# Performance work log

Hardware: AMD Instinct MI355X
Metric: run time of the kernel (lower is better)

Reference implementation:

```python
import jax, jax.numpy as jnp
import numpy as np

T = 15          # fixed window length from docstring
CENTER = 7      # center_idx
MAXL = 8        # max_len_f = max_len_b = 8
B, D, H = 8192, 512, 512


def _gru_final(x, lengths, Wih, Whh, bih, bhh):
    """Run a GRU over x (B, L, D) and return the hidden state after each
    sample's own `lengths` steps (packed-sequence final-hidden semantics)."""
    Bn, L, _ = x.shape
    Hn = Whh.shape[1]
    # Precompute input projections for all timesteps: (B, L, 3H)
    xp = jnp.einsum('bld,gd->blg', x, Wih) + bih
    mask = jnp.arange(L)[None, :] < lengths[:, None]  # (B, L) valid steps

    def step(h, inp):
        xp_t, m_t = inp                      # (B,3H), (B,)
        gh = h @ Whh.T + bhh                 # (B,3H)
        xr, xz, xn = jnp.split(xp_t, 3, axis=-1)
        hr, hz, hn = jnp.split(gh, 3, axis=-1)
        r = jax.nn.sigmoid(xr + hr)
        z = jax.nn.sigmoid(xz + hz)
        n = jnp.tanh(xn + r * hn)
        h_new = (1.0 - z) * n + z * h
        h = jnp.where(m_t[:, None], h_new, h)  # freeze h past sequence end
        return h, None

    h0 = jnp.zeros((Bn, Hn), x.dtype)
    hT, _ = jax.lax.scan(step, h0, (jnp.moveaxis(xp, 0, 1)[:L], mask.T))
    return hT


def setup_inputs() -> dict:
    key = jax.random.key(0)
    ks = jax.random.split(key, 16)
    s_ih = 1.0 / np.sqrt(H)
    u = lambda k, shape: jax.random.uniform(k, shape, jnp.float32, -s_ih, s_ih)
    inp = {
        'padded_window': jax.random.normal(ks[0], (B, T, D), jnp.float32),
        'window_len': jax.random.randint(ks[1], (B,), 1, T + 1, jnp.int32),
        # forward GRU params (PyTorch layout: gates ordered r,z,n)
        'Wih_f': u(ks[2], (3 * H, D)), 'Whh_f': u(ks[3], (3 * H, H)),
        'bih_f': u(ks[4], (3 * H,)),   'bhh_f': u(ks[5], (3 * H,)),
        # backward GRU params
        'Wih_b': u(ks[6], (3 * H, D)), 'Whh_b': u(ks[7], (3 * H, H)),
        'bih_b': u(ks[8], (3 * H,)),   'bhh_b': u(ks[9], (3 * H,)),
        # MLP: Linear(2H,H) -> ReLU -> Linear(H,H)
        'W1': u(ks[10], (H, 2 * H)), 'b1': u(ks[11], (H,)),
        'W2': u(ks[12], (H, H)),     'b2': u(ks[13], (H,)),
    }
    return inp


def reference(padded_window, window_len, Wih_f, Whh_f, bih_f, bhh_f,
              Wih_b, Whh_b, bih_b, bhh_b, W1, b1, W2, b2):
    len_f = (window_len - 1) // 2 + 1   # (B,)
    len_b = window_len // 2 + 1         # (B,)
    j = jnp.arange(MAXL)
    # forward sub-sequence: window[center-l_f+1 : center+1]
    idx_f = jnp.clip(CENTER - len_f[:, None] + 1 + j[None, :], 0, T - 1)
    # backward sub-sequence: flip(window[center : center+l_b]) -> descending idx
    idx_b = jnp.clip(CENTER + len_b[:, None] - 1 - j[None, :], 0, T - 1)
    xf = jnp.take_along_axis(padded_window, idx_f[:, :, None], axis=1)  # (B,8,D)
    xb = jnp.take_along_axis(padded_window, idx_b[:, :, None], axis=1)  # (B,8,D)
    h_f = _gru_final(xf, len_f, Wih_f, Whh_f, bih_f, bhh_f)
    h_b = _gru_final(xb, len_b, Wih_b, Whh_b, bih_b, bhh_b)
    combined = jnp.concatenate([h_f, h_b], axis=1)  # (B, 2H)
    hidden = jax.nn.relu(combined @ W1.T + b1)
    return hidden @ W2.T + b2
```

## Files before the change

kernel.cpp:

```cpp
#include <hip/hip_runtime.h>

typedef unsigned short u16;
typedef __attribute__((ext_vector_type(4))) float f32x4;
typedef __attribute__((ext_vector_type(8))) __bf16 bf16x8;
typedef __attribute__((ext_vector_type(8))) u16 u16x8;
typedef __attribute__((ext_vector_type(4))) u16 u16x4;
typedef __attribute__((ext_vector_type(4))) int i32x4;

#define MFMA(a, b, c) __builtin_amdgcn_mfma_f32_16x16x32_bf16(a, b, c, 0, 0, 0)

__device__ __forceinline__ u16 f2bf(float f) {
  union { float f; unsigned u; } v; v.f = f;
  unsigned r = v.u + 0x7FFFu + ((v.u >> 16) & 1u);
  return (u16)(r >> 16);
}
__device__ __forceinline__ float bf2f(u16 b) {
  union { unsigned u; float f; } v; v.u = ((unsigned)b) << 16; return v.f;
}
__device__ __forceinline__ float sigm(float x) { return 1.f / (1.f + __expf(-x)); }
__device__ __forceinline__ float tanh_(float x) {
  float e = __expf(-2.f * fabsf(x));
  float r = (1.f - e) / (1.f + e);
  return x < 0.f ? -r : r;
}

#define GSTRIDE 131072

__global__ __launch_bounds__(256) void cvt_bf16(const float* __restrict__ src,
                                                u16* __restrict__ dst, int n8) {
  int i = blockIdx.x * 256 + threadIdx.x;
  if (i >= n8) return;
  int e = i * 8;
  u16x8 o;
#pragma unroll
  for (int j = 0; j < 8; ++j) o[j] = f2bf(src[e + j]);
  *(u16x8*)(dst + e) = o;
}

#define LROWA 520

__global__ __launch_bounds__(256)
__attribute__((amdgpu_waves_per_eu(1, 1))) void xp_gemm(
    const float* __restrict__ win, const int* __restrict__ wlen,
    const u16* __restrict__ Wihb_f, const u16* __restrict__ Wihb_b,
    const float* __restrict__ bih_f, const float* __restrict__ bih_b,
    const float* __restrict__ bhh_f, const float* __restrict__ bhh_b,
    u16* __restrict__ xp) {
  extern __shared__ char smem[];
  u16* As = (u16*)smem;

  const int dir = blockIdx.y;
  const u16* Wb = dir ? Wihb_b : Wihb_f;
  const float* bih = dir ? bih_b : bih_f;
  const float* bhh = dir ? bhh_b : bhh_f;

  const int tid = threadIdx.x;
  const int bx = blockIdx.x;

  {
    const int r = tid >> 1, hh = tid & 1;
    const int m = bx * 128 + r;
    const int s = m >> 3, tt = m & 7;
    const int wl = wlen[s];
    const int len = dir ? (wl / 2 + 1) : ((wl - 1) / 2 + 1);
    const int widx = dir ? (6 + len - tt) : (8 - len + tt);
    const float* src = win + ((size_t)s * 15 + widx) * 512 + hh * 256;
    u16* dst = As + r * LROWA + hh * 256;
#pragma unroll
    for (int i = 0; i < 32; ++i) {
      f32x4 v0 = *(const f32x4*)(src + i * 8);
      f32x4 v1 = *(const f32x4*)(src + i * 8 + 4);
      u16x8 o;
      o[0] = f2bf(v0[0]); o[1] = f2bf(v0[1]); o[2] = f2bf(v0[2]); o[3] = f2bf(v0[3]);
      o[4] = f2bf(v1[0]); o[5] = f2bf(v1[1]); o[6] = f2bf(v1[2]); o[7] = f2bf(v1[3]);
      *(u16x8*)(dst + i * 8) = o;
    }
  }
  __syncthreads();

  const int wave = tid >> 6;
  const int lane = tid & 63;
  const int ln = lane & 15;
  const int ks = lane >> 4;

#pragma unroll 1
  for (int g = 0; g < 6; ++g) {
    const int c0 = wave * 24 + g * 4;

    f32x4 acc[8][4];
#pragma unroll
    for (int mt = 0; mt < 8; ++mt)
#pragma unroll
      for (int u = 0; u < 4; ++u)
#pragma unroll
        for (int j = 0; j < 4; ++j) acc[mt][u][j] = 0.f;

#pragma unroll
    for (int kk = 0; kk < 16; ++kk) {
      const int krel = kk * 32 + ks * 8;
      bf16x8 a[8];
#pragma unroll
      for (int mt = 0; mt < 8; ++mt)
        a[mt] = *(const bf16x8*)(As + (mt * 16 + ln) * LROWA + krel);
      bf16x8 b[4];
#pragma unroll
      for (int u = 0; u < 4; ++u)
        b[u] = *(const bf16x8*)(Wb + (size_t)((c0 + u) * 16 + ln) * 512 + krel);
#pragma unroll
      for (int mt = 0; mt < 8; ++mt)
#pragma unroll
        for (int u = 0; u < 4; ++u) acc[mt][u] = MFMA(a[mt], b[u], acc[mt][u]);
    }

#pragma unroll
    for (int u = 0; u < 4; ++u) {
      const int col = (c0 + u) * 16 + ln;
      const float bv = bih[col] + (col < 1024 ? bhh[col] : 0.f);
#pragma unroll
      for (int mt = 0; mt < 8; ++mt)
#pragma unroll
        for (int j = 0; j < 4; ++j) {
          const int rowm = bx * 128 + mt * 16 + ks * 4 + j;
          const int s = rowm >> 3, t = rowm & 7;
          const size_t idx = ((size_t)(dir * 8 + t) * 96 + (c0 + u)) * GSTRIDE +
                             (size_t)(s >> 2) * 64 + ln * 4 + (s & 3);
          xp[idx] = f2bf(acc[mt][u][j] + bv);
        }
    }
  }
}

#define LROW 520

__global__ __launch_bounds__(1024)
__attribute__((amdgpu_waves_per_eu(4, 4))) void gru_rec(
    const int* __restrict__ wlen, const u16* __restrict__ Whhb_f,
    const u16* __restrict__ Whhb_b, const float* __restrict__ bhh_f,
    const float* __restrict__ bhh_b, const u16* __restrict__ xp,
    u16* __restrict__ hcat) {
  extern __shared__ char smem[];
  u16* hb0 = (u16*)smem;
  u16* hb1 = hb0 + 64 * LROW;
  int* len_s = (int*)(hb1 + 64 * LROW);
  int* bmax_s = len_s + 64;

  const int dir = blockIdx.x & 1;
  const int grp = blockIdx.x >> 1;
  const int s0 = grp * 64;
  const u16* W = dir ? Whhb_b : Whhb_f;
  const float* bhh = dir ? bhh_b : bhh_f;

  const int tid = threadIdx.x;
  const int wave = tid >> 6;
  const int lane = tid & 63;
  const int ln = lane & 15;
  const int ks = lane >> 4;

  if (tid == 0) *bmax_s = 0;
  for (int i = tid; i < 64 * LROW / 8; i += 1024) ((u16x8*)hb0)[i] = (u16x8)0;
  __syncthreads();
  if (tid < 64) {
    int wl = wlen[s0 + tid];
    int len = dir ? (wl / 2 + 1) : ((wl - 1) / 2 + 1);
    len_s[tid] = len;
    atomicMax(bmax_s, len);
  }
  __syncthreads();
  const int bmax = *bmax_s;

  float b_hn[2];
#pragma unroll
  for (int p = 0; p < 2; ++p) b_hn[p] = bhh[1024 + (p * 16 + wave) * 16 + ln];

  for (int t = 0; t < bmax; ++t) {
    u16* h_cur = (t & 1) ? hb1 : hb0;
    u16* h_nxt = (t & 1) ? hb0 : hb1;
    const u16* xpt = xp + (size_t)(dir * 8 + t) * 96 * GSTRIDE;

#pragma unroll
    for (int p = 0; p < 2; ++p) {
      const int q = p * 16 + wave;
      const int dcol = q * 16 + ln;
      const u16* wrow = W + (size_t)dcol * 512;

      u16x4 xr4[4], xz4[4], xn4[4];
#pragma unroll
      for (int mt = 0; mt < 4; ++mt) {
        const size_t off = (size_t)((s0 >> 2) + mt * 4 + ks) * 64 + ln * 4;
        xr4[mt] = *(const u16x4*)(xpt + (size_t)q * GSTRIDE + off);
        xz4[mt] = *(const u16x4*)(xpt + (size_t)(32 + q) * GSTRIDE + off);
        xn4[mt] = *(const u16x4*)(xpt + (size_t)(64 + q) * GSTRIDE + off);
      }

      f32x4 accr[4], accz[4], acchn[4];
#pragma unroll
      for (int mt = 0; mt < 4; ++mt)
#pragma unroll
        for (int j = 0; j < 4; ++j) {
          accr[mt][j] = 0.f; accz[mt][j] = 0.f; acchn[mt][j] = 0.f;
        }

#pragma unroll
      for (int kk = 0; kk < 16; ++kk) {
        const int krel = kk * 32 + ks * 8;
        bf16x8 a[4];
#pragma unroll
        for (int mt = 0; mt < 4; ++mt)
          a[mt] = *(const bf16x8*)(h_cur + (mt * 16 + ln) * LROW + krel);
        bf16x8 br = *(const bf16x8*)(wrow + krel);
        bf16x8 bz = *(const bf16x8*)(wrow + 512 * 512 + krel);
        bf16x8 bn = *(const bf16x8*)(wrow + 1024 * 512 + krel);
#pragma unroll
        for (int mt = 0; mt < 4; ++mt) {
          accr[mt] = MFMA(a[mt], br, accr[mt]);
          accz[mt] = MFMA(a[mt], bz, accz[mt]);
          acchn[mt] = MFMA(a[mt], bn, acchn[mt]);
        }
      }

#pragma unroll
      for (int mt = 0; mt < 4; ++mt)
#pragma unroll
        for (int j = 0; j < 4; ++j) {
          const int row = mt * 16 + ks * 4 + j;
          float xr = bf2f(xr4[mt][j]);
          float xz = bf2f(xz4[mt][j]);
          float xn = bf2f(xn4[mt][j]);
          float rr = sigm(accr[mt][j] + xr);
          float zz = sigm(accz[mt][j] + xz);
          float nn = tanh_(xn + rr * (acchn[mt][j] + b_hn[p]));
          float hold = bf2f(h_cur[row * LROW + dcol]);
          float hnew = (t < len_s[row]) ? ((1.f - zz) * nn + zz * hold) : hold;
          h_nxt[row * LROW + dcol] = f2bf(hnew);
        }
    }
    __syncthreads();
  }

  const u16* hf = (bmax & 1) ? hb1 : hb0;
  const int xrow = tid >> 4;
  const int xcol = tid & 15;
#pragma unroll
  for (int i = 0; i < 4; ++i) {
    int off = (i * 16 + xcol) * 8;
    u16x8 v = *(const u16x8*)(hf + xrow * LROW + off);
    __builtin_nontemporal_store(
        v, (u16x8*)(hcat + (size_t)(s0 + xrow) * 1024 + dir * 512 + off));
  }
}

__global__ __launch_bounds__(256) void build_wcat(const float* __restrict__ Whh,
                                                  const float* __restrict__ Wih,
                                                  u16* __restrict__ Wcat) {
  int i = blockIdx.x * 256 + threadIdx.x;
  if (i >= 1536 * 1024 / 8) return;
  int e = i * 8;
  int g = e >> 10, k = e & 1023;
  const float* src = (k < 512) ? (Whh + g * 512 + k) : (Wih + g * 512 + (k - 512));
  u16x8 o;
#pragma unroll
  for (int j = 0; j < 8; ++j) o[j] = f2bf(src[j]);
  *(u16x8*)(Wcat + e) = o;
}

__global__ __launch_bounds__(512)
__attribute__((amdgpu_waves_per_eu(2, 2))) void gru_persistent(
    const float* __restrict__ win, const int* __restrict__ wlen,
    const u16* __restrict__ Wcat_f, const u16* __restrict__ Wcat_b,
    const float* __restrict__ bih_f, const float* __restrict__ bhh_f,
    const float* __restrict__ bih_b, const float* __restrict__ bhh_b,
    u16* __restrict__ hcat) {
  extern __shared__ char smem[];
  u16* h_s = (u16*)smem;
  u16* x_s = (u16*)(smem + 64 * LROW * 2);
  int* len_s = (int*)(smem + 2 * 64 * LROW * 2);
  int* bmax_s = len_s + 64;

  const int dir = blockIdx.x & 1;
  const int grp = blockIdx.x >> 1;
  const int s0 = grp * 64;
  const u16* W = dir ? Wcat_b : Wcat_f;
  const float* bih = dir ? bih_b : bih_f;
  const float* bhh = dir ? bhh_b : bhh_f;

  const int tid = threadIdx.x;
  const int wave = tid >> 6;
  const int lane = tid & 63;
  const int ln = lane & 15;
  const int ks = lane >> 4;

  if (tid == 0) *bmax_s = 0;
  for (int i = tid; i < 64 * LROW / 8; i += 512) ((u16x8*)h_s)[i] = (u16x8)0;
  __syncthreads();
  if (tid < 64) {
    int wl = wlen[s0 + tid];
    int len = dir ? (wl / 2 + 1) : ((wl - 1) / 2 + 1);
    len_s[tid] = len;
    atomicMax(bmax_s, len);
  }
  __syncthreads();
  const int bmax = *bmax_s;

  float b_r[4], b_z[4], b_xn[4], b_hn[4];
#pragma unroll
  for (int p = 0; p < 4; ++p) {
    int d = (p * 8 + wave) * 16 + ln;
    b_r[p] = bih[d] + bhh[d];
    b_z[p] = bih[512 + d] + bhh[512 + d];
    b_xn[p] = bih[1024 + d];
    b_hn[p] = bhh[1024 + d];
  }

  const int xrow = tid >> 3;
  const int xcol = tid & 7;
  const int mylen = len_s[xrow];
  const long xbase = (long)(s0 + xrow) * 15 + (dir ? (6 + mylen) : (8 - mylen));

  for (int t = 0; t < bmax; ++t) {
    {
      long rowidx = dir ? (xbase - t) : (xbase + t);
      const float* src = win + rowidx * 512;
      u16* dst = x_s + xrow * LROW;
#pragma unroll
      for (int i = 0; i < 8; ++i) {
        int off = xcol * 8 + i * 64;
        f32x4 v0 = *(const f32x4*)(src + off);
        f32x4 v1 = *(const f32x4*)(src + off + 4);
        u16x8 o;
        o[0] = f2bf(v0[0]); o[1] = f2bf(v0[1]); o[2] = f2bf(v0[2]); o[3] = f2bf(v0[3]);
        o[4] = f2bf(v1[0]); o[5] = f2bf(v1[1]); o[6] = f2bf(v1[2]); o[7] = f2bf(v1[3]);
        *(u16x8*)(dst + off) = o;
      }
    }
    __syncthreads();

    unsigned holdp[3][4][2];

#pragma unroll
    for (int p = 0; p < 4; ++p) {
      const int dcol = (p * 8 + wave) * 16 + ln;
      const u16* wrow = W + (size_t)dcol * 1024;

      f32x4 accr[4], accz[4], acchn[4], accxn[4];
#pragma unroll
      for (int mt = 0; mt < 4; ++mt)
#pragma unroll
        for (int j = 0; j < 4; ++j) {
          accr[mt][j] = 0.f; accz[mt][j] = 0.f;
          acchn[mt][j] = 0.f; accxn[mt][j] = 0.f;
        }

#pragma unroll
      for (int kk = 0; kk < 16; ++kk) {
        const int krel = kk * 32 + ks * 8;
        bf16x8 a[4];
#pragma unroll
        for (int mt = 0; mt < 4; ++mt)
          a[mt] = *(const bf16x8*)(h_s + (mt * 16 + ln) * LROW + krel);
        bf16x8 br = *(const bf16x8*)(wrow + krel);
        bf16x8 bz = *(const bf16x8*)(wrow + 512 * 1024 + krel);
        bf16x8 bn = *(const bf16x8*)(wrow + 1024 * 1024 + krel);
#pragma unroll
        for (int mt = 0; mt < 4; ++mt) {
          accr[mt] = MFMA(a[mt], br, accr[mt]);
          accz[mt] = MFMA(a[mt], bz, accz[mt]);
          acchn[mt] = MFMA(a[mt], bn, acchn[mt]);
        }
      }
#pragma unroll
      for (int kk = 0; kk < 16; ++kk) {
        const int krel = kk * 32 + ks * 8;
        bf16x8 a[4];
#pragma unroll
        for (int mt = 0; mt < 4; ++mt)
          a[mt] = *(const bf16x8*)(x_s + (mt * 16 + ln) * LROW + krel);
        bf16x8 br = *(const bf16x8*)(wrow + 512 + krel);
        bf16x8 bz = *(const bf16x8*)(wrow + 512 * 1024 + 512 + krel);
        bf16x8 bn = *(const bf16x8*)(wrow + 1024 * 1024 + 512 + krel);
#pragma unroll
        for (int mt = 0; mt < 4; ++mt) {
          accr[mt] = MFMA(a[mt], br, accr[mt]);
          accz[mt] = MFMA(a[mt], bz, accz[mt]);
          accxn[mt] = MFMA(a[mt], bn, accxn[mt]);
        }
      }

      if (p < 3) {
#pragma unroll
        for (int mt = 0; mt < 4; ++mt)
#pragma unroll
          for (int jp = 0; jp < 2; ++jp) {
            unsigned pk = 0;
#pragma unroll
            for (int jh = 0; jh < 2; ++jh) {
              const int j = jp * 2 + jh;
              const int row = mt * 16 + ks * 4 + j;
              float rr = sigm(accr[mt][j] + b_r[p]);
              float zz = sigm(accz[mt][j] + b_z[p]);
              float nn = tanh_(accxn[mt][j] + b_xn[p] +
                               rr * (acchn[mt][j] + b_hn[p]));
              float hold = bf2f(h_s[row * LROW + dcol]);
              float hnew = (t < len_s[row]) ? ((1.f - zz) * nn + zz * hold) : hold;
              pk |= ((unsigned)f2bf(hnew)) << (16 * jh);
            }
            holdp[p][mt][jp] = pk;
          }
      } else {
        __syncthreads();
#pragma unroll
        for (int pp = 0; pp < 3; ++pp) {
          const int dd = (pp * 8 + wave) * 16 + ln;
#pragma unroll
          for (int mt = 0; mt < 4; ++mt)
#pragma unroll
            for (int jp = 0; jp < 2; ++jp) {
              unsigned pk = holdp[pp][mt][jp];
              const int row = mt * 16 + ks * 4 + jp * 2;
              h_s[row * LROW + dd] = (u16)pk;
              h_s[(row + 1) * LROW + dd] = (u16)(pk >> 16);
            }
        }
#pragma unroll
        for (int mt = 0; mt < 4; ++mt)
#pragma unroll
          for (int j = 0; j < 4; ++j) {
            const int row = mt * 16 + ks * 4 + j;
            float rr = sigm(accr[mt][j] + b_r[3]);
            float zz = sigm(accz[mt][j] + b_z[3]);
            float nn = tanh_(accxn[mt][j] + b_xn[3] +
                             rr * (acchn[mt][j] + b_hn[3]));
            float hold = bf2f(h_s[row * LROW + dcol]);
            float hnew = (t < len_s[row]) ? ((1.f - zz) * nn + zz * hold) : hold;
            h_s[row * LROW + dcol] = f2bf(hnew);
          }
      }
    }
  }

  __syncthreads();
#pragma unroll
  for (int i = 0; i < 8; ++i) {
    int off = xcol * 8 + i * 64;
    u16x8 v = *(const u16x8*)(h_s + xrow * LROW + off);
    __builtin_nontemporal_store(
        v, (u16x8*)(hcat + (size_t)(s0 + xrow) * 1024 + dir * 512 + off));
  }
}

__global__ __launch_bounds__(256) void mlp_gemm(const u16* __restrict__ A,
                                                const u16* __restrict__ Bw,
                                                const float* __restrict__ bias,
                                                void* __restrict__ out, int M,
                                                int N, int K, int mode) {
  __shared__ u16 As[128 * 64], Bs[128 * 64];
  const int tid = threadIdx.x;
  const int wave = tid >> 6, lane = tid & 63;
  const int ln = lane & 15, ks = lane >> 4;
  const int wm = wave & 1, wn = wave >> 1;
  const int m0 = blockIdx.x * 128, n0 = blockIdx.y * 128;
  f32x4 acc[4][4];
#pragma unroll
  for (int mt = 0; mt < 4; ++mt)
#pragma unroll
    for (int nt = 0; nt < 4; ++nt)
#pragma unroll
      for (int j = 0; j < 4; ++j) acc[mt][nt][j] = 0.f;

  const int r = tid >> 1, hh = tid & 1;
  for (int k0 = 0; k0 < K; k0 += 64) {
    const i32x4* sa = (const i32x4*)(A + (size_t)(m0 + r) * K + k0 + hh * 32);
    const i32x4* sb = (const i32x4*)(Bw + (size_t)(n0 + r) * K + k0 + hh * 32);
    i32x4* da = (i32x4*)(As + r * 64 + hh * 32);
    i32x4* db = (i32x4*)(Bs + r * 64 + hh * 32);
#pragma unroll
    for (int i = 0; i < 4; ++i) da[i] = sa[i];
#pragma unroll
    for (int i = 0; i < 4; ++i) db[i] = sb[i];
    __syncthreads();
#pragma unroll
    for (int kk = 0; kk < 2; ++kk) {
      bf16x8 af[4], bfm[4];
#pragma unroll
      for (int mt = 0; mt < 4; ++mt)
        af[mt] = *(const bf16x8*)(As + (wm * 64 + mt * 16 + ln) * 64 + kk * 32 + ks * 8);
#pragma unroll
      for (int nt = 0; nt < 4; ++nt)
        bfm[nt] = *(const bf16x8*)(Bs + (wn * 64 + nt * 16 + ln) * 64 + kk * 32 + ks * 8);
#pragma unroll
      for (int mt = 0; mt < 4; ++mt)
#pragma unroll
        for (int nt = 0; nt < 4; ++nt) acc[mt][nt] = MFMA(af[mt], bfm[nt], acc[mt][nt]);
    }
    __syncthreads();
  }

#pragma unroll
  for (int nt = 0; nt < 4; ++nt) {
    int col = n0 + wn * 64 + nt * 16 + ln;
    float bv = bias[col];
#pragma unroll
    for (int mt = 0; mt < 4; ++mt)
#pragma unroll
      for (int j = 0; j < 4; ++j) {
        int row = m0 + wm * 64 + mt * 16 + ks * 4 + j;
        float v = acc[mt][nt][j] + bv;
        if (mode) {
          v = fmaxf(v, 0.f);
          ((u16*)out)[(size_t)row * N + col] = f2bf(v);
        } else {
          ((float*)out)[(size_t)row * N + col] = v;
        }
      }
  }
}

extern "C" void kernel_launch(void* const* d_in, const int* in_sizes, int n_in,
                              void* d_out, int out_size, void* d_ws, size_t ws_size,
                              hipStream_t stream) {
  (void)in_sizes; (void)n_in; (void)out_size;
  const float* win = (const float*)d_in[0];
  const int* wlen = (const int*)d_in[1];
  const float* Wih_f = (const float*)d_in[2];
  const float* Whh_f = (const float*)d_in[3];
  const float* bih_f = (const float*)d_in[4];
  const float* bhh_f = (const float*)d_in[5];
  const float* Wih_b = (const float*)d_in[6];
  const float* Whh_b = (const float*)d_in[7];
  const float* bih_b = (const float*)d_in[8];
  const float* bhh_b = (const float*)d_in[9];
  const float* W1 = (const float*)d_in[10];
  const float* b1 = (const float*)d_in[11];
  const float* W2 = (const float*)d_in[12];
  const float* b2 = (const float*)d_in[13];

  const size_t NEED = 4ull * 1572864 + 1048576 + 524288 + 16777216 + 8388608 +
                      402653184ull;

  if (ws_size >= NEED) {
    char* ws = (char*)d_ws;
    u16* Whhb_f = (u16*)ws; ws += 1572864;
    u16* Whhb_b = (u16*)ws; ws += 1572864;
    u16* Wihb_f = (u16*)ws; ws += 1572864;
    u16* Wihb_b = (u16*)ws; ws += 1572864;
    u16* W1b = (u16*)ws;    ws += 1048576;
    u16* W2b = (u16*)ws;    ws += 524288;
    u16* hcat = (u16*)ws;   ws += 16777216;
    u16* hidden = (u16*)ws; ws += 8388608;
    u16* xp = (u16*)ws;     ws += 402653184;

    cvt_bf16<<<384, 256, 0, stream>>>(Whh_f, Whhb_f, 98304);
    cvt_bf16<<<384, 256, 0, stream>>>(Whh_b, Whhb_b, 98304);
    cvt_bf16<<<384, 256, 0, stream>>>(Wih_f, Wihb_f, 98304);
    cvt_bf16<<<384, 256, 0, stream>>>(Wih_b, Wihb_b, 98304);
    cvt_bf16<<<256, 256, 0, stream>>>(W1, W1b, 65536);
    cvt_bf16<<<128, 256, 0, stream>>>(W2, W2b, 32768);

    const int SMEM_XP = 128 * LROWA * 2;
    (void)hipFuncSetAttribute((const void*)xp_gemm,
                              hipFuncAttributeMaxDynamicSharedMemorySize, SMEM_XP);
    xp_gemm<<<dim3(512, 2), 256, SMEM_XP, stream>>>(
        win, wlen, Wihb_f, Wihb_b, bih_f, bih_b, bhh_f, bhh_b, xp);

    const int SMEM = 2 * 64 * LROW * 2 + 64 * 4 + 16;
    (void)hipFuncSetAttribute((const void*)gru_rec,
                              hipFuncAttributeMaxDynamicSharedMemorySize, SMEM);
    gru_rec<<<256, 1024, SMEM, stream>>>(wlen, Whhb_f, Whhb_b, bhh_f, bhh_b, xp,
                                         hcat);

    mlp_gemm<<<dim3(64, 4), 256, 0, stream>>>(hcat, W1b, b1, hidden, 8192, 512, 1024, 1);
    mlp_gemm<<<dim3(64, 4), 256, 0, stream>>>(hidden, W2b, b2, d_out, 8192, 512, 512, 0);
  } else {
    char* ws = (char*)d_ws;
    u16* Wcat_f = (u16*)ws;  ws += 3145728;
    u16* Wcat_b = (u16*)ws;  ws += 3145728;
    u16* W1b = (u16*)ws;     ws += 1048576;
    u16* W2b = (u16*)ws;     ws += 524288;
    u16* hcat = (u16*)ws;    ws += 16777216;
    u16* hidden = (u16*)ws;  ws += 8388608;

    build_wcat<<<768, 256, 0, stream>>>(Whh_f, Wih_f, Wcat_f);
    build_wcat<<<768, 256, 0, stream>>>(Whh_b, Wih_b, Wcat_b);
    cvt_bf16<<<256, 256, 0, stream>>>(W1, W1b, 65536);
    cvt_bf16<<<128, 256, 0, stream>>>(W2, W2b, 32768);

    const int SMEM = 2 * 64 * LROW * 2 + 64 * 4 + 16;
    (void)hipFuncSetAttribute((const void*)gru_persistent,
                              hipFuncAttributeMaxDynamicSharedMemorySize, SMEM);
    gru_persistent<<<256, 512, SMEM, stream>>>(win, wlen, Wcat_f, Wcat_b, bih_f,
                                               bhh_f, bih_b, bhh_b, hcat);

    mlp_gemm<<<dim3(64, 4), 256, 0, stream>>>(hcat, W1b, b1, hidden, 8192, 512, 1024, 1);
    mlp_gemm<<<dim3(64, 4), 256, 0, stream>>>(hidden, W2b, b2, d_out, 8192, 512, 512, 0);
  }
}
```

Measured before the change: 1.885 ms.

## Sort samples by length and repack recurrent weights into MFMA fragment order

Adds a counting sort of samples by window length so each GRU block and input-projection block holds samples of similar length. The projection GEMM is reorganised per timestep and skips tiles whose longest sample has already finished, and the recurrence's per-block step count shrinks. The final MLP scatters rows back through the permutation. Separately, Whh is repacked so each wave's B-fragment loads are contiguous and coalesced, at the cost of an extra sort kernel and indirect indexing.

```diff
diff --git a/kernel.cpp b/kernel.cpp
--- a/kernel.cpp
+++ b/kernel.cpp
@@ -37,34 +37,81 @@
   *(u16x8*)(dst + e) = o;
 }
 
+__global__ __launch_bounds__(256) void wrepack(const float* __restrict__ Whh,
+                                               u16* __restrict__ Wp) {
+  int i = blockIdx.x * 256 + threadIdx.x;
+  if (i >= 98304) return;
+  int q = i / 3072;
+  int r1 = i % 3072;
+  int kk = r1 / 192;
+  int r2 = r1 % 192;
+  int g = r2 / 64;
+  int r3 = r2 % 64;
+  int ks = r3 >> 4, ln = r3 & 15;
+  const float* src =
+      Whh + (size_t)(g * 512 + q * 16 + ln) * 512 + kk * 32 + ks * 8;
+  u16x8 o;
+#pragma unroll
+  for (int j = 0; j < 8; ++j) o[j] = f2bf(src[j]);
+  *(u16x8*)(Wp + (size_t)i * 8) = o;
+}
+
+__global__ __launch_bounds__(1024) void sort_len(const int* __restrict__ wlen,
+                                                 int* __restrict__ order) {
+  __shared__ int cnt[16];
+  __shared__ int off[16];
+  const int tid = threadIdx.x;
+  if (tid < 16) cnt[tid] = 0;
+  __syncthreads();
+  for (int i = tid; i < 8192; i += 1024) atomicAdd(&cnt[wlen[i] - 1], 1);
+  __syncthreads();
+  if (tid == 0) {
+    int run = 0;
+#pragma unroll
+    for (int b = 0; b < 15; ++b) { off[b] = run; run += cnt[b]; }
+  }
+  __syncthreads();
+  for (int i = tid; i < 8192; i += 1024) {
+    int pos = atomicAdd(&off[wlen[i] - 1], 1);
+    order[pos] = i;
+  }
+}
+
 #define LROWA 520
 
 __global__ __launch_bounds__(256)
 __attribute__((amdgpu_waves_per_eu(1, 1))) void xp_gemm(
     const float* __restrict__ win, const int* __restrict__ wlen,
-    const u16* __restrict__ Wihb_f, const u16* __restrict__ Wihb_b,
-    const float* __restrict__ bih_f, const float* __restrict__ bih_b,
-    const float* __restrict__ bhh_f, const float* __restrict__ bhh_b,
-    u16* __restrict__ xp) {
+    const int* __restrict__ order, const u16* __restrict__ Wihb_f,
+    const u16* __restrict__ Wihb_b, const float* __restrict__ bih_f,
+    const float* __restrict__ bih_b, const float* __restrict__ bhh_f,
+    const float* __restrict__ bhh_b, u16* __restrict__ xp) {
   extern __shared__ char smem[];
   u16* As = (u16*)smem;
 
-  const int dir = blockIdx.y;
+  const int dir = blockIdx.z;
+  const int t = blockIdx.y;
+  const int sbase = blockIdx.x * 128;
+
+  {
+    int wl_last = wlen[order[sbase + 127]];
+    int len_last = dir ? (wl_last / 2 + 1) : ((wl_last - 1) / 2 + 1);
+    if (len_last <= t) return;
+  }
+
   const u16* Wb = dir ? Wihb_b : Wihb_f;
   const float* bih = dir ? bih_b : bih_f;
   const float* bhh = dir ? bhh_b : bhh_f;
 
   const int tid = threadIdx.x;
-  const int bx = blockIdx.x;
 
   {
     const int r = tid >> 1, hh = tid & 1;
-    const int m = bx * 128 + r;
-    const int s = m >> 3, tt = m & 7;
-    const int wl = wlen[s];
+    const int sample = order[sbase + r];
+    const int wl = wlen[sample];
     const int len = dir ? (wl / 2 + 1) : ((wl - 1) / 2 + 1);
-    const int widx = dir ? (6 + len - tt) : (8 - len + tt);
-    const float* src = win + ((size_t)s * 15 + widx) * 512 + hh * 256;
+    const int widx = dir ? (6 + len - t) : (8 - len + t);
+    const float* src = win + ((size_t)sample * 15 + widx) * 512 + hh * 256;
     u16* dst = As + r * LROWA + hh * 256;
 #pragma unroll
     for (int i = 0; i < 32; ++i) {
@@ -120,10 +167,9 @@
       for (int mt = 0; mt < 8; ++mt)
 #pragma unroll
         for (int j = 0; j < 4; ++j) {
-          const int rowm = bx * 128 + mt * 16 + ks * 4 + j;
-          const int s = rowm >> 3, t = rowm & 7;
+          const int slot = sbase + mt * 16 + ks * 4 + j;
           const size_t idx = ((size_t)(dir * 8 + t) * 96 + (c0 + u)) * GSTRIDE +
-                             (size_t)(s >> 2) * 64 + ln * 4 + (s & 3);
+                             (size_t)(slot >> 2) * 64 + ln * 4 + (slot & 3);
           xp[idx] = f2bf(acc[mt][u][j] + bv);
         }
     }
@@ -134,10 +180,10 @@
 
 __global__ __launch_bounds__(1024)
 __attribute__((amdgpu_waves_per_eu(4, 4))) void gru_rec(
-    const int* __restrict__ wlen, const u16* __restrict__ Whhb_f,
-    const u16* __restrict__ Whhb_b, const float* __restrict__ bhh_f,
-    const float* __restrict__ bhh_b, const u16* __restrict__ xp,
-    u16* __restrict__ hcat) {
+    const int* __restrict__ wlen, const int* __restrict__ order,
+    const u16* __restrict__ Wp_f, const u16* __restrict__ Wp_b,
+    const float* __restrict__ bhh_f, const float* __restrict__ bhh_b,
+    const u16* __restrict__ xp, u16* __restrict__ hcat) {
   extern __shared__ char smem[];
   u16* hb0 = (u16*)smem;
   u16* hb1 = hb0 + 64 * LROW;
@@ -147,7 +193,7 @@
   const int dir = blockIdx.x & 1;
   const int grp = blockIdx.x >> 1;
   const int s0 = grp * 64;
-  const u16* W = dir ? Whhb_b : Whhb_f;
+  const u16* W = dir ? Wp_b : Wp_f;
   const float* bhh = dir ? bhh_b : bhh_f;
 
   const int tid = threadIdx.x;
@@ -160,7 +206,7 @@
   for (int i = tid; i < 64 * LROW / 8; i += 1024) ((u16x8*)hb0)[i] = (u16x8)0;
   __syncthreads();
   if (tid < 64) {
-    int wl = wlen[s0 + tid];
+    int wl = wlen[order[s0 + tid]];
     int len = dir ? (wl / 2 + 1) : ((wl - 1) / 2 + 1);
     len_s[tid] = len;
     atomicMax(bmax_s, len);
@@ -181,7 +227,7 @@
     for (int p = 0; p < 2; ++p) {
       const int q = p * 16 + wave;
       const int dcol = q * 16 + ln;
-      const u16* wrow = W + (size_t)dcol * 512;
+      const u16* wq = W + (size_t)q * 24576 + lane * 8;
 
       u16x4 xr4[4], xz4[4], xn4[4];
 #pragma unroll
@@ -207,9 +253,10 @@
 #pragma unroll
         for (int mt = 0; mt < 4; ++mt)
           a[mt] = *(const bf16x8*)(h_cur + (mt * 16 + ln) * LROW + krel);
-        bf16x8 br = *(const bf16x8*)(wrow + krel);
-        bf16x8 bz = *(const bf16x8*)(wrow + 512 * 512 + krel);
-        bf16x8 bn = *(const bf16x8*)(wrow + 1024 * 512 + krel);
+        const u16* wk = wq + kk * 1536;
+        bf16x8 br = *(const bf16x8*)(wk);
+        bf16x8 bz = *(const bf16x8*)(wk + 512);
+        bf16x8 bn = *(const bf16x8*)(wk + 1024);
 #pragma unroll
         for (int mt = 0; mt < 4; ++mt) {
           accr[mt] = MFMA(a[mt], br, accr[mt]);
@@ -450,6 +497,7 @@
 __global__ __launch_bounds__(256) void mlp_gemm(const u16* __restrict__ A,
                                                 const u16* __restrict__ Bw,
                                                 const float* __restrict__ bias,
+                                                const int* __restrict__ perm,
                                                 void* __restrict__ out, int M,
                                                 int N, int K, int mode) {
   __shared__ u16 As[128 * 64], Bs[128 * 64];
@@ -504,11 +552,12 @@
       for (int j = 0; j < 4; ++j) {
         int row = m0 + wm * 64 + mt * 16 + ks * 4 + j;
         float v = acc[mt][nt][j] + bv;
+        int orow = perm ? perm[row] : row;
         if (mode) {
           v = fmaxf(v, 0.f);
-          ((u16*)out)[(size_t)row * N + col] = f2bf(v);
+          ((u16*)out)[(size_t)orow * N + col] = f2bf(v);
         } else {
-          ((float*)out)[(size_t)row * N + col] = v;
+          ((float*)out)[(size_t)orow * N + col] = v;
         }
       }
   }
@@ -534,22 +583,24 @@
   const float* b2 = (const float*)d_in[13];
 
   const size_t NEED = 4ull * 1572864 + 1048576 + 524288 + 16777216 + 8388608 +
-                      402653184ull;
+                      402653184ull + 32768;
 
   if (ws_size >= NEED) {
     char* ws = (char*)d_ws;
-    u16* Whhb_f = (u16*)ws; ws += 1572864;
-    u16* Whhb_b = (u16*)ws; ws += 1572864;
+    u16* Wp_f = (u16*)ws;   ws += 1572864;
+    u16* Wp_b = (u16*)ws;   ws += 1572864;
     u16* Wihb_f = (u16*)ws; ws += 1572864;
     u16* Wihb_b = (u16*)ws; ws += 1572864;
     u16* W1b = (u16*)ws;    ws += 1048576;
     u16* W2b = (u16*)ws;    ws += 524288;
     u16* hcat = (u16*)ws;   ws += 16777216;
     u16* hidden = (u16*)ws; ws += 8388608;
+    int* order = (int*)ws;  ws += 32768;
     u16* xp = (u16*)ws;     ws += 402653184;
 
-    cvt_bf16<<<384, 256, 0, stream>>>(Whh_f, Whhb_f, 98304);
-    cvt_bf16<<<384, 256, 0, stream>>>(Whh_b, Whhb_b, 98304);
+    sort_len<<<1, 1024, 0, stream>>>(wlen, order);
+    wrepack<<<384, 256, 0, stream>>>(Whh_f, Wp_f);
+    wrepack<<<384, 256, 0, stream>>>(Whh_b, Wp_b);
     cvt_bf16<<<384, 256, 0, stream>>>(Wih_f, Wihb_f, 98304);
     cvt_bf16<<<384, 256, 0, stream>>>(Wih_b, Wihb_b, 98304);
     cvt_bf16<<<256, 256, 0, stream>>>(W1, W1b, 65536);
@@ -558,17 +609,19 @@
     const int SMEM_XP = 128 * LROWA * 2;
     (void)hipFuncSetAttribute((const void*)xp_gemm,
                               hipFuncAttributeMaxDynamicSharedMemorySize, SMEM_XP);
-    xp_gemm<<<dim3(512, 2), 256, SMEM_XP, stream>>>(
-        win, wlen, Wihb_f, Wihb_b, bih_f, bih_b, bhh_f, bhh_b, xp);
+    xp_gemm<<<dim3(64, 8, 2), 256, SMEM_XP, stream>>>(
+        win, wlen, order, Wihb_f, Wihb_b, bih_f, bih_b, bhh_f, bhh_b, xp);
 
     const int SMEM = 2 * 64 * LROW * 2 + 64 * 4 + 16;
     (void)hipFuncSetAttribute((const void*)gru_rec,
                               hipFuncAttributeMaxDynamicSharedMemorySize, SMEM);
-    gru_rec<<<256, 1024, SMEM, stream>>>(wlen, Whhb_f, Whhb_b, bhh_f, bhh_b, xp,
-                                         hcat);
-
-    mlp_gemm<<<dim3(64, 4), 256, 0, stream>>>(hcat, W1b, b1, hidden, 8192, 512, 1024, 1);
-    mlp_gemm<<<dim3(64, 4), 256, 0, stream>>>(hidden, W2b, b2, d_out, 8192, 512, 512, 0);
+    gru_rec<<<256, 1024, SMEM, stream>>>(wlen, order, Wp_f, Wp_b, bhh_f, bhh_b,
+                                         xp, hcat);
+
+    mlp_gemm<<<dim3(64, 4), 256, 0, stream>>>(hcat, W1b, b1, nullptr, hidden,
+                                              8192, 512, 1024, 1);
+    mlp_gemm<<<dim3(64, 4), 256, 0, stream>>>(hidden, W2b, b2, order, d_out,
+                                              8192, 512, 512, 0);
   } else {
     char* ws = (char*)d_ws;
     u16* Wcat_f = (u16*)ws;  ws += 3145728;
@@ -589,7 +642,9 @@
     gru_persistent<<<256, 512, SMEM, stream>>>(win, wlen, Wcat_f, Wcat_b, bih_f,
                                                bhh_f, bih_b, bhh_b, hcat);
 
-    mlp_gemm<<<dim3(64, 4), 256, 0, stream>>>(hcat, W1b, b1, hidden, 8192, 512, 1024, 1);
-    mlp_gemm<<<dim3(64, 4), 256, 0, stream>>>(hidden, W2b, b2, d_out, 8192, 512, 512, 0);
-  }
-}
+    mlp_gemm<<<dim3(64, 4), 256, 0, stream>>>(hcat, W1b, b1, nullptr, hidden,
+                                              8192, 512, 1024, 1);
+    mlp_gemm<<<dim3(64, 4), 256, 0, stream>>>(hidden, W2b, b2, nullptr, d_out,
+                                              8192, 512, 512, 0);
+  }
+}
```

Result: slower. 1.947 ms (+3.3%).
